# Optimization experiments

Measured on AMD Instinct MI355X. Metric: run time of the kernel, lower is better.

Reference implementation:

```python
import jax, jax.numpy as jnp
import numpy as np

NEG = -1e30  # safe -inf surrogate (keeps grads finite)
BLANK = 0
PRIOR_SCALE = 0.3


def prior_logsumexp(log_probs, input_lengths):
    # log_probs: [T, N, V]; logsumexp over all valid (t, n) frames -> [1, V]
    T = log_probs.shape[0]
    mask = jnp.arange(T)[:, None] < input_lengths[None, :]  # [T, N]
    masked = jnp.where(mask[:, :, None], log_probs, NEG)
    return jax.nn.logsumexp(masked, axis=(0, 1))[None, :]


def ctc_loss_mean(log_probs, targets, input_lengths, target_lengths):
    # Exact CTC forward (alpha) recursion, vectorized over batch, scanned over time.
    # log_probs: [T, N, V] (log scores), targets: [N, S] with values >= 1.
    T, N, V = log_probs.shape
    S = targets.shape[1]
    L = 2 * S + 1  # extended label sequence with interleaved blanks
    ext = jnp.full((N, L), BLANK, dtype=targets.dtype).at[:, 1::2].set(targets)
    # skip transition j-2 -> j allowed iff ext[j] != blank and ext[j] != ext[j-2]
    skip = jnp.zeros((N, L), bool).at[:, 2:].set(
        (ext[:, 2:] != BLANK) & (ext[:, 2:] != ext[:, :-2]))
    pad1 = jnp.full((N, 1), NEG, log_probs.dtype)
    pad2 = jnp.full((N, 2), NEG, log_probs.dtype)

    e0 = jnp.take_along_axis(log_probs[0], ext, axis=1)  # [N, L]
    alpha0 = (jnp.full((N, L), NEG, log_probs.dtype)
              .at[:, 0].set(e0[:, 0])
              .at[:, 1].set(e0[:, 1]))

    def step(alpha, xs):
        lp_t, t = xs
        emit = jnp.take_along_axis(lp_t, ext, axis=1)  # [N, L]
        s1 = jnp.concatenate([pad1, alpha[:, :-1]], axis=1)
        s2 = jnp.where(skip, jnp.concatenate([pad2, alpha[:, :-2]], axis=1), NEG)
        new = jax.nn.logsumexp(jnp.stack([alpha, s1, s2], 0), axis=0) + emit
        # freeze finished utterances (t >= input_length)
        alpha = jnp.where((t < input_lengths)[:, None], new, alpha)
        return alpha, None

    alpha, _ = jax.lax.scan(step, alpha0, (log_probs[1:], jnp.arange(1, T)))

    i1 = (2 * target_lengths)[:, None]
    a1 = jnp.take_along_axis(alpha, i1, axis=1)[:, 0]
    a2 = jnp.take_along_axis(alpha, i1 - 1, axis=1)[:, 0]
    ll = jnp.logaddexp(a1, a2)  # total log-likelihood per utterance
    # k2.ctc_loss(reduction='mean', target_lengths=...) == mean of (-ll / target_len)
    return jnp.mean(-ll / target_lengths.astype(log_probs.dtype))


def setup_inputs() -> dict:
    key = jax.random.key(0)
    k1, k2, k3, k4, k5 = jax.random.split(key, 5)
    T, N, V, S = 2000, 32, 256, 256
    log_probs = jax.nn.log_softmax(jax.random.normal(k1, (T, N, V), jnp.float32), axis=-1)
    log_priors = jax.nn.log_softmax(0.5 * jax.random.normal(k2, (1, V), jnp.float32), axis=-1)
    targets = jax.random.randint(k3, (N, S), 1, V)          # non-blank labels
    input_lengths = jax.random.randint(k4, (N,), T // 2, T + 1)
    target_lengths = jax.random.randint(k5, (N,), S // 2, S + 1)
    return {"log_probs": log_probs, "log_priors": log_priors, "targets": targets,
            "input_lengths": input_lengths, "target_lengths": target_lengths}


def reference(log_probs, log_priors, targets, input_lengths, target_lengths):
    # (1) detached label-prior accumulation pass (as in training step)
    log_batch_priors_sum = jax.lax.stop_gradient(prior_logsumexp(log_probs, input_lengths))
    # (2) prior-scaled log probs (log_priors broadcasts [1,V] -> [T,N,V])
    scaled = log_probs - PRIOR_SCALE * log_priors
    # (3) CTC forward-backward loss
    loss = ctc_loss_mean(scaled, targets, input_lengths, target_lengths)
    return loss, log_batch_priors_sum
```

## Files before the change

### kernel.cpp

```cpp
#include <hip/hip_runtime.h>

#define PRIOR_SCALE 0.3f
#define NEGF (-1e30f)
#define LOG2E_F 1.4426950408889634f
#define LN2_F 0.6931471805599453f
#define K_SS 8
#define MARG 24

#define PHASE_BARRIER() \
  asm volatile("s_waitcnt lgkmcnt(0)\n\ts_barrier" ::: "memory")

__device__ __forceinline__ float fexp2(float x) { return __builtin_amdgcn_exp2f(x); }
__device__ __forceinline__ float flog2(float x) { return __builtin_amdgcn_logf(x); }

__device__ __forceinline__ float lse2b(float a, float b) {
  float m = fmaxf(a, b);
  float d = fminf(a, b) - m;
  return m + flog2(1.0f + fexp2(d));
}

__device__ __forceinline__ float shr1_dpp(float x, float fill) {
  return __int_as_float(__builtin_amdgcn_update_dpp(
      __float_as_int(fill), __float_as_int(x), 0x138 , 0xF, 0xF, false));
}
__device__ __forceinline__ int shr1_dpp_i(int x, int fill) {
  return __builtin_amdgcn_update_dpp(fill, x, 0x138, 0xF, 0xF, false);
}
template <int CTRL, int RM>
__device__ __forceinline__ int dppi(int x) {
  return __builtin_amdgcn_update_dpp(x, x, CTRL, RM, 0xF, false);
}
__device__ __forceinline__ int imax2(int a, int b) { return a > b ? a : b; }

__device__ __forceinline__ void issue_pair(float& e, float& b, uint32_t offE,
                                           uint32_t offB, uint64_t base) {
  asm volatile("global_load_dword %0, %2, %4\n\t"
               "global_load_dword %1, %3, %4"
               : "=v"(e), "=v"(b)
               : "v"(offE), "v"(offB), "s"(base));
}
__device__ __forceinline__ void wait_pair(float& e, float& b) {
  asm volatile("s_waitcnt vmcnt(14)" : "+v"(e), "+v"(b));
}

extern "C" __global__ void __launch_bounds__(256, 1)
ctc_fused_kernel(const float* __restrict__ lp, const float* __restrict__ lpri,
                 const int* __restrict__ tgt, const int* __restrict__ ilen,
                 const int* __restrict__ tlen, float* __restrict__ nll,
                 float* __restrict__ partial, int pblocks,
                 int T, int N, int V, int S) {
  if ((int)blockIdx.x >= N) {
    const int pb = blockIdx.x - N;
    const int v = threadIdx.x;
    float s = 0.0f;
    for (int t = pb; t < T; t += pblocks) {
      const float* base = lp + (size_t)t * N * V + v;
      for (int nn = 0; nn < N; ++nn) {
        float x = base[(size_t)nn * V];
        s += (t < ilen[nn]) ? __expf(x) : 0.0f;
      }
    }
    partial[(size_t)pb * V + v] = s;
    return;
  }

  const int n = blockIdx.x;
  const int g = threadIdx.x;
  const int lane = g & 63;
  const int wid = __builtin_amdgcn_readfirstlane(threadIdx.x >> 6);
  __shared__ __align__(16) float mb[3][2048];
  __shared__ int mbe[3][256];
  __shared__ float afin[513];

  const int len = __builtin_amdgcn_readfirstlane(ilen[n]);
  const int tl = tlen[n];

  const int* trow = tgt + n * S;
  const int tv = trow[g];
  const int tvp = (g > 0) ? trow[g - 1] : -1;
  const float skf = (g > 0 && tv != tvp) ? 1.0f : 0.0f;
  const float ep1 = (-PRIOR_SCALE * lpri[tv]) * LOG2E_F;
  const float epb = (-PRIOR_SCALE * lpri[0]) * LOG2E_F;
  const int penB = MARG * ((lane & 15) + 1);
  const int penC = MARG * ((lane & 31) + 1);

  const float* rp = lp + (size_t)n * V;
  const uint32_t RBu = (uint32_t)(N * V * 4);
  const uint32_t tvb = (uint32_t)tv * 4u;
  const uint64_t gbase = (uint64_t)(uintptr_t)rp;

  float x0 = 0.0f, x1 = 0.0f, x2 = 0.0f;
  int e = 0;
  { float b0 = rp[0], e0 = rp[tv];
    if (g == 0) {
      x0 = fexp2(fmaf(b0, LOG2E_F, epb));
      x1 = fexp2(fmaf(e0, LOG2E_F, ep1));
    } }
  for (int idx = g; idx < 3 * 2048; idx += 256) ((float*)mb)[idx] = 0.0f;
  for (int idx = g; idx < 3 * 256; idx += 256) ((int*)mbe)[idx] = 0;

  float eR0, eR1, eR2, eR3, eR4, eR5, eR6, eR7;
  float bR0, bR1, bR2, bR3, bR4, bR5, bR6, bR7;
#define PRO(K) { uint32_t tt = (uint32_t)((1 + K < len) ? (1 + K) : (len - 1)); \
                 issue_pair(eR##K, bR##K, tt * RBu + tvb, tt * RBu, gbase); }
  PRO(0) PRO(1) PRO(2) PRO(3) PRO(4) PRO(5) PRO(6) PRO(7)
#undef PRO
  uint32_t ofB;
  { uint32_t tn = (uint32_t)((1 + K_SS < len) ? (1 + K_SS) : (len - 1));
    ofB = tn * RBu; }

  float mv0 = 0, mv1 = 0, mv2 = 0, mv3 = 0, mv4 = 0, mv5 = 0, mv6 = 0, mv7 = 0;

  PHASE_BARRIER();

  const int nss = (len - 1 + K_SS - 1) / K_SS;
  const int P = nss + 3;

#define STEP(KK, T_, DSC_) {                                                   \
    const int t = (T_);                                                        \
    if (t < len) {                                                             \
      wait_pair(eR##KK, bR##KK);                                               \
      float e1  = fexp2(fmaf(eR##KK, LOG2E_F, ep1));                           \
      float ebl = fexp2(fmaf(bR##KK, LOG2E_F, epb));                           \
      issue_pair(eR##KK, bR##KK, ofB + tvb, ofB, gbase);                       \
      ofB += ((t + 1 + K_SS) < len) ? RBu : 0u;                                \
      float am1 = ldexpf(shr1_dpp(x1, mv##KK), (DSC_));                        \
      am1 = fminf(am1, 1.0e33f);                         \
      float sel = (g == 255) ? x1 : 0.0f;                                      \
      float y0 = (x0 + am1) * ebl;                                             \
      float y1 = fmaf(skf, am1, x1 + x0) * e1;                                 \
      x2 = (x2 + sel) * ebl;                                                   \
      x0 = y0; x1 = y1;                                                        \
      if (lane == 63 && wid < 3) mb[wid][t] = y1;       \
    } }

  for (int p = 0; p < P; ++p) {
    const int i = p - wid;
    if (i >= 0 && i < nss) {
      const int t0 = 1 + i * K_SS;
      int eA = 0, eB = 0;
      if (wid > 0) {
        eB = mbe[wid - 1][i];
        eA = (i > 0) ? mbe[wid - 1][i - 1] : eB;
        const float4* mrow = (const float4*)&mb[wid - 1][t0 - 1];
        float4 q0 = mrow[0], q1 = mrow[1];
        mv0 = q0.x; mv1 = q0.y; mv2 = q0.z; mv3 = q0.w;
        mv4 = q1.x; mv5 = q1.y; mv6 = q1.z; mv7 = q1.w;
      }
      int dscL, dsc0;
      {
        float mxv = fmaxf(fmaxf(x0, x1), x2);
        int ex = (int)((__float_as_uint(mxv) >> 23) & 0xFFu) - 127;
        int ecand = (mxv > 0.0f) ? (e + ex - 40) : -2000000;
        if (wid > 0 && lane == 0) ecand = imax2(ecand, imax2(eA, eB) - MARG);
        int v = ecand;
        v = imax2(v, dppi<0x111, 0xF>(v) - MARG);
        v = imax2(v, dppi<0x112, 0xF>(v) - 2 * MARG);
        v = imax2(v, dppi<0x114, 0xF>(v) - 4 * MARG);
        v = imax2(v, dppi<0x118, 0xF>(v) - 8 * MARG);
        v = imax2(v, dppi<0x142, 0xA>(v) - penB);
        v = imax2(v, dppi<0x143, 0xC>(v) - penC);
        int dsc = e - v;
        x0 = ldexpf(x0, dsc);
        x1 = ldexpf(x1, dsc);
        x2 = ldexpf(x2, dsc);
        e = v;
        if (lane == 63 && wid < 3) mbe[wid][i] = e;
        int eprevL = shr1_dpp_i(e, eB);
        dscL = eprevL - e;
        dsc0 = (lane == 0) ? (eA - e) : dscL;
      }
      STEP(0, t0 + 0, dsc0)  STEP(1, t0 + 1, dscL)
      STEP(2, t0 + 2, dscL)  STEP(3, t0 + 3, dscL)
      STEP(4, t0 + 4, dscL)  STEP(5, t0 + 5, dscL)
      STEP(6, t0 + 6, dscL)  STEP(7, t0 + 7, dscL)
    }
    PHASE_BARRIER();
  }
#undef STEP

  asm volatile("s_waitcnt vmcnt(0)");
  asm volatile("" :: "v"(eR0), "v"(eR1), "v"(eR2), "v"(eR3),
                     "v"(eR4), "v"(eR5), "v"(eR6), "v"(eR7));
  asm volatile("" :: "v"(bR0), "v"(bR1), "v"(bR2), "v"(bR3),
                     "v"(bR4), "v"(bR5), "v"(bR6), "v"(bR7));

  const float ef = (float)e;
  afin[2 * g]     = fmaxf(flog2(x0) + ef, NEGF);
  afin[2 * g + 1] = fmaxf(flog2(x1) + ef, NEGF);
  if (g == 255) afin[512] = fmaxf(flog2(x2) + ef, NEGF);
  __syncthreads();
  if (g == 0) {
    const int i1 = 2 * tl;
    float ll = lse2b(afin[i1], afin[i1 - 1]) * LN2_F;
    nll[n] = -ll / (float)tl;
  }
}

extern "C" __global__ void finalize_kernel(const float* __restrict__ partial, int nstripes,
                                           const float* __restrict__ nll,
                                           float* __restrict__ out, int N, int V) {
  const int v = threadIdx.x;
  float s = 0.0f;
#pragma unroll 4
  for (int pb = 0; pb < nstripes; ++pb) s += partial[(size_t)pb * V + v];
  out[1 + v] = __logf(s);
  if (v == 0) {
    float acc = 0.0f;
#pragma unroll 8
    for (int i = 0; i < N; ++i) acc += nll[i];
    out[0] = acc / (float)N;
  }
}

extern "C" void kernel_launch(void* const* d_in, const int* in_sizes, int n_in,
                              void* d_out, int out_size, void* d_ws, size_t ws_size,
                              hipStream_t stream) {
  const float* lp   = (const float*)d_in[0];
  const float* lpri = (const float*)d_in[1];
  const int*   tgt  = (const int*)d_in[2];
  const int*   ilen = (const int*)d_in[3];
  const int*   tlen = (const int*)d_in[4];
  const int V = in_sizes[1];
  const int N = in_sizes[3];
  const int S = in_sizes[2] / N;
  const int T = in_sizes[0] / (N * V);

  int pblocks = 200;
  size_t need = ((size_t)pblocks * V + 64) * sizeof(float);
  if (ws_size < need) {
    long avail = (long)(ws_size / sizeof(float)) - 64;
    pblocks = (int)(avail / V);
    if (pblocks < 1) pblocks = 1;
  }

  float* out = (float*)d_out;
  float* partial = (float*)d_ws;
  float* nll = partial + (size_t)pblocks * V;

  ctc_fused_kernel<<<N + pblocks, 256, 0, stream>>>(lp, lpri, tgt, ilen, tlen,
                                                    nll, partial, pblocks, T, N, V, S);
  finalize_kernel<<<1, 256, 0, stream>>>(partial, pblocks, nll, out, N, V);
}
```

Measured before the change: 221.9 us.

## Precompute gathered emission exponentials in a parallel prep kernel before the serial scan

Adds a prep kernel that gathers the target-label and blank log-probs for every (n, t) and applies the prior scaling and exp2, storing them in a contiguous per-utterance workspace layout. The same kernel also does the prior logsumexp partial sums. The serial scan kernel then reads coalesced, precomputed emissions instead of doing strided gathers and exps on its critical path. The cost is an extra kernel launch and a large workspace write and read (N*T*256 floats), plus a two-stage finalize. The old fused kernel is kept as a fallback for when the workspace is too small.

```diff
diff --git a/kernel.cpp b/kernel.cpp
--- a/kernel.cpp
+++ b/kernel.cpp
@@ -6,6 +6,7 @@
 #define LN2_F 0.6931471805599453f
 #define K_SS 8
 #define MARG 24
+#define PB 512
 
 #define PHASE_BARRIER() \
   asm volatile("s_waitcnt lgkmcnt(0)\n\ts_barrier" ::: "memory")
@@ -43,27 +44,45 @@
   asm volatile("s_waitcnt vmcnt(14)" : "+v"(e), "+v"(b));
 }
 
+extern "C" __global__ void __launch_bounds__(256)
+prep_kernel(const float* __restrict__ lp, const float* __restrict__ lpri,
+            const int* __restrict__ tgt, const int* __restrict__ ilen,
+            float* __restrict__ Eodd, float* __restrict__ Ebl,
+            float* __restrict__ partial, int T, int N, int V, int S) {
+  const int tid = threadIdx.x;
+  const int b = blockIdx.x;
+  __shared__ int   stv[32 * 256];
+  __shared__ float spe[32 * 256];
+  __shared__ int   slen[32];
+  for (int idx = tid; idx < N * 256; idx += 256) {
+    int vv = tgt[idx];
+    stv[idx] = vv;
+    spe[idx] = (-PRIOR_SCALE * lpri[vv]) * LOG2E_F;
+  }
+  if (tid < N) slen[tid] = ilen[tid];
+  const float epb = (-PRIOR_SCALE * lpri[0]) * LOG2E_F;
+  __syncthreads();
+
+  float psum = 0.0f;
+  for (int t = b; t < T; t += PB) {
+#pragma unroll 2
+    for (int n = 0; n < 32; ++n) {
+      const float* row = lp + ((size_t)t * N + n) * V;
+      float val = row[tid];
+      if (t < slen[n]) psum += __expf(val);
+      float ev = row[stv[n * 256 + tid]];
+      Eodd[((size_t)n * T + t) * 256 + tid] =
+          fexp2(fmaf(ev, LOG2E_F, spe[n * 256 + tid]));
+      if (tid == 0) Ebl[(size_t)n * T + t] = fexp2(fmaf(row[0], LOG2E_F, epb));
+    }
+  }
+  partial[(size_t)b * 256 + tid] = psum;
+}
+
 extern "C" __global__ void __launch_bounds__(256, 1)
-ctc_fused_kernel(const float* __restrict__ lp, const float* __restrict__ lpri,
-                 const int* __restrict__ tgt, const int* __restrict__ ilen,
-                 const int* __restrict__ tlen, float* __restrict__ nll,
-                 float* __restrict__ partial, int pblocks,
-                 int T, int N, int V, int S) {
-  if ((int)blockIdx.x >= N) {
-    const int pb = blockIdx.x - N;
-    const int v = threadIdx.x;
-    float s = 0.0f;
-    for (int t = pb; t < T; t += pblocks) {
-      const float* base = lp + (size_t)t * N * V + v;
-      for (int nn = 0; nn < N; ++nn) {
-        float x = base[(size_t)nn * V];
-        s += (t < ilen[nn]) ? __expf(x) : 0.0f;
-      }
-    }
-    partial[(size_t)pb * V + v] = s;
-    return;
-  }
-
+ctc_scan_kernel(const float* __restrict__ ws_f, const int* __restrict__ tgt,
+                const int* __restrict__ ilen, const int* __restrict__ tlen,
+                float* __restrict__ nll, int T, int N, int S) {
   const int n = blockIdx.x;
   const int g = threadIdx.x;
   const int lane = g & 63;
@@ -79,35 +98,32 @@
   const int tv = trow[g];
   const int tvp = (g > 0) ? trow[g - 1] : -1;
   const float skf = (g > 0 && tv != tvp) ? 1.0f : 0.0f;
-  const float ep1 = (-PRIOR_SCALE * lpri[tv]) * LOG2E_F;
-  const float epb = (-PRIOR_SCALE * lpri[0]) * LOG2E_F;
   const int penB = MARG * ((lane & 15) + 1);
   const int penC = MARG * ((lane & 31) + 1);
 
-  const float* rp = lp + (size_t)n * V;
-  const uint32_t RBu = (uint32_t)(N * V * 4);
-  const uint32_t tvb = (uint32_t)tv * 4u;
-  const uint64_t gbase = (uint64_t)(uintptr_t)rp;
+  const float* eoddn = ws_f + (size_t)n * T * 256;
+  const uint64_t gbase = (uint64_t)(uintptr_t)eoddn;
+  const uint32_t eblOffB = (uint32_t)((((size_t)(N - n) * T) * 256 + (size_t)n * T) * 4);
+  const uint32_t gb4 = (uint32_t)g * 4u;
 
   float x0 = 0.0f, x1 = 0.0f, x2 = 0.0f;
   int e = 0;
-  { float b0 = rp[0], e0 = rp[tv];
-    if (g == 0) {
-      x0 = fexp2(fmaf(b0, LOG2E_F, epb));
-      x1 = fexp2(fmaf(e0, LOG2E_F, ep1));
-    } }
+  if (g == 0) {
+    x0 = ws_f[(size_t)N * T * 256 + (size_t)n * T];
+    x1 = eoddn[0];
+  }
   for (int idx = g; idx < 3 * 2048; idx += 256) ((float*)mb)[idx] = 0.0f;
   for (int idx = g; idx < 3 * 256; idx += 256) ((int*)mbe)[idx] = 0;
 
   float eR0, eR1, eR2, eR3, eR4, eR5, eR6, eR7;
   float bR0, bR1, bR2, bR3, bR4, bR5, bR6, bR7;
 #define PRO(K) { uint32_t tt = (uint32_t)((1 + K < len) ? (1 + K) : (len - 1)); \
-                 issue_pair(eR##K, bR##K, tt * RBu + tvb, tt * RBu, gbase); }
+                 issue_pair(eR##K, bR##K, tt * 1024u + gb4, eblOffB + tt * 4u, gbase); }
   PRO(0) PRO(1) PRO(2) PRO(3) PRO(4) PRO(5) PRO(6) PRO(7)
 #undef PRO
-  uint32_t ofB;
+  uint32_t ofE, ofBl;
   { uint32_t tn = (uint32_t)((1 + K_SS < len) ? (1 + K_SS) : (len - 1));
-    ofB = tn * RBu; }
+    ofE = tn * 1024u; ofBl = eblOffB + tn * 4u; }
 
   float mv0 = 0, mv1 = 0, mv2 = 0, mv3 = 0, mv4 = 0, mv5 = 0, mv6 = 0, mv7 = 0;
 
@@ -120,10 +136,12 @@
     const int t = (T_);                                                        \
     if (t < len) {                                                             \
       wait_pair(eR##KK, bR##KK);                                               \
-      float e1  = fexp2(fmaf(eR##KK, LOG2E_F, ep1));                           \
-      float ebl = fexp2(fmaf(bR##KK, LOG2E_F, epb));                           \
-      issue_pair(eR##KK, bR##KK, ofB + tvb, ofB, gbase);                       \
-      ofB += ((t + 1 + K_SS) < len) ? RBu : 0u;                                \
+      float e1  = eR##KK;                                                      \
+      float ebl = bR##KK;                                                      \
+      issue_pair(eR##KK, bR##KK, ofE + gb4, ofBl, gbase);                      \
+      bool adv = ((t + 1 + K_SS) < len);                                       \
+      ofE  += adv ? 1024u : 0u;                                                \
+      ofBl += adv ? 4u : 0u;                                                   \
       float am1 = ldexpf(shr1_dpp(x1, mv##KK), (DSC_));                        \
       am1 = fminf(am1, 1.0e33f);                         \
       float sel = (g == 255) ? x1 : 0.0f;                                      \
@@ -197,6 +215,171 @@
   }
 }
 
+extern "C" __global__ void __launch_bounds__(256)
+finalize1_kernel(const float* __restrict__ partial, float* __restrict__ partial2) {
+  const int v = threadIdx.x;
+  const int b = blockIdx.x;
+  float s = 0.0f;
+#pragma unroll 4
+  for (int pb = b; pb < PB; pb += 32) s += partial[(size_t)pb * 256 + v];
+  partial2[(size_t)b * 256 + v] = s;
+}
+extern "C" __global__ void __launch_bounds__(256)
+finalize2_kernel(const float* __restrict__ partial2, const float* __restrict__ nll,
+                 float* __restrict__ out, int N) {
+  const int v = threadIdx.x;
+  float s = 0.0f;
+#pragma unroll
+  for (int b = 0; b < 32; ++b) s += partial2[(size_t)b * 256 + v];
+  out[1 + v] = __logf(s);
+  if (v == 0) {
+    float acc = 0.0f;
+#pragma unroll 8
+    for (int i = 0; i < N; ++i) acc += nll[i];
+    out[0] = acc / (float)N;
+  }
+}
+
+extern "C" __global__ void __launch_bounds__(256, 1)
+ctc_fused_r12(const float* __restrict__ lp, const float* __restrict__ lpri,
+              const int* __restrict__ tgt, const int* __restrict__ ilen,
+              const int* __restrict__ tlen, float* __restrict__ nll,
+              float* __restrict__ partial, int pblocks,
+              int T, int N, int V, int S) {
+  if ((int)blockIdx.x >= N) {
+    const int pb = blockIdx.x - N;
+    const int v = threadIdx.x;
+    float s = 0.0f;
+    for (int t = pb; t < T; t += pblocks) {
+      const float* base = lp + (size_t)t * N * V + v;
+      for (int nn = 0; nn < N; ++nn) {
+        float x = base[(size_t)nn * V];
+        s += (t < ilen[nn]) ? __expf(x) : 0.0f;
+      }
+    }
+    partial[(size_t)pb * V + v] = s;
+    return;
+  }
+  const int n = blockIdx.x;
+  const int g = threadIdx.x;
+  const int lane = g & 63;
+  const int wid = __builtin_amdgcn_readfirstlane(threadIdx.x >> 6);
+  __shared__ __align__(16) float mb[3][2048];
+  __shared__ int mbe[3][256];
+  __shared__ float afin[513];
+  const int len = __builtin_amdgcn_readfirstlane(ilen[n]);
+  const int tl = tlen[n];
+  const int* trow = tgt + n * S;
+  const int tv = trow[g];
+  const int tvp = (g > 0) ? trow[g - 1] : -1;
+  const float skf = (g > 0 && tv != tvp) ? 1.0f : 0.0f;
+  const float ep1 = (-PRIOR_SCALE * lpri[tv]) * LOG2E_F;
+  const float epb = (-PRIOR_SCALE * lpri[0]) * LOG2E_F;
+  const int penB = MARG * ((lane & 15) + 1);
+  const int penC = MARG * ((lane & 31) + 1);
+  const float* rp = lp + (size_t)n * V;
+  const uint32_t RBu = (uint32_t)(N * V * 4);
+  const uint32_t tvb = (uint32_t)tv * 4u;
+  const uint64_t gbase = (uint64_t)(uintptr_t)rp;
+  float x0 = 0.0f, x1 = 0.0f, x2 = 0.0f;
+  int e = 0;
+  { float b0 = rp[0], e0 = rp[tv];
+    if (g == 0) {
+      x0 = fexp2(fmaf(b0, LOG2E_F, epb));
+      x1 = fexp2(fmaf(e0, LOG2E_F, ep1));
+    } }
+  for (int idx = g; idx < 3 * 2048; idx += 256) ((float*)mb)[idx] = 0.0f;
+  for (int idx = g; idx < 3 * 256; idx += 256) ((int*)mbe)[idx] = 0;
+  float eR0, eR1, eR2, eR3, eR4, eR5, eR6, eR7;
+  float bR0, bR1, bR2, bR3, bR4, bR5, bR6, bR7;
+#define PRO(K) { uint32_t tt = (uint32_t)((1 + K < len) ? (1 + K) : (len - 1)); \
+                 issue_pair(eR##K, bR##K, tt * RBu + tvb, tt * RBu, gbase); }
+  PRO(0) PRO(1) PRO(2) PRO(3) PRO(4) PRO(5) PRO(6) PRO(7)
+#undef PRO
+  uint32_t ofB;
+  { uint32_t tn = (uint32_t)((1 + K_SS < len) ? (1 + K_SS) : (len - 1));
+    ofB = tn * RBu; }
+  float mv0 = 0, mv1 = 0, mv2 = 0, mv3 = 0, mv4 = 0, mv5 = 0, mv6 = 0, mv7 = 0;
+  PHASE_BARRIER();
+  const int nss = (len - 1 + K_SS - 1) / K_SS;
+  const int P = nss + 3;
+#define STEP(KK, T_, DSC_) {                                                   \
+    const int t = (T_);                                                        \
+    if (t < len) {                                                             \
+      wait_pair(eR##KK, bR##KK);                                               \
+      float e1  = fexp2(fmaf(eR##KK, LOG2E_F, ep1));                           \
+      float ebl = fexp2(fmaf(bR##KK, LOG2E_F, epb));                           \
+      issue_pair(eR##KK, bR##KK, ofB + tvb, ofB, gbase);                       \
+      ofB += ((t + 1 + K_SS) < len) ? RBu : 0u;                                \
+      float am1 = ldexpf(shr1_dpp(x1, mv##KK), (DSC_));                        \
+      am1 = fminf(am1, 1.0e33f);                                               \
+      float sel = (g == 255) ? x1 : 0.0f;                                      \
+      float y0 = (x0 + am1) * ebl;                                             \
+      float y1 = fmaf(skf, am1, x1 + x0) * e1;                                 \
+      x2 = (x2 + sel) * ebl;                                                   \
+      x0 = y0; x1 = y1;                                                        \
+      if (lane == 63 && wid < 3) mb[wid][t] = y1;                              \
+    } }
+  for (int p = 0; p < P; ++p) {
+    const int i = p - wid;
+    if (i >= 0 && i < nss) {
+      const int t0 = 1 + i * K_SS;
+      int eA = 0, eB = 0;
+      if (wid > 0) {
+        eB = mbe[wid - 1][i];
+        eA = (i > 0) ? mbe[wid - 1][i - 1] : eB;
+        const float4* mrow = (const float4*)&mb[wid - 1][t0 - 1];
+        float4 q0 = mrow[0], q1 = mrow[1];
+        mv0 = q0.x; mv1 = q0.y; mv2 = q0.z; mv3 = q0.w;
+        mv4 = q1.x; mv5 = q1.y; mv6 = q1.z; mv7 = q1.w;
+      }
+      int dscL, dsc0;
+      {
+        float mxv = fmaxf(fmaxf(x0, x1), x2);
+        int ex = (int)((__float_as_uint(mxv) >> 23) & 0xFFu) - 127;
+        int ecand = (mxv > 0.0f) ? (e + ex - 40) : -2000000;
+        if (wid > 0 && lane == 0) ecand = imax2(ecand, imax2(eA, eB) - MARG);
+        int v = ecand;
+        v = imax2(v, dppi<0x111, 0xF>(v) - MARG);
+        v = imax2(v, dppi<0x112, 0xF>(v) - 2 * MARG);
+        v = imax2(v, dppi<0x114, 0xF>(v) - 4 * MARG);
+        v = imax2(v, dppi<0x118, 0xF>(v) - 8 * MARG);
+        v = imax2(v, dppi<0x142, 0xA>(v) - penB);
+        v = imax2(v, dppi<0x143, 0xC>(v) - penC);
+        int dsc = e - v;
+        x0 = ldexpf(x0, dsc);
+        x1 = ldexpf(x1, dsc);
+        x2 = ldexpf(x2, dsc);
+        e = v;
+        if (lane == 63 && wid < 3) mbe[wid][i] = e;
+        int eprevL = shr1_dpp_i(e, eB);
+        dscL = eprevL - e;
+        dsc0 = (lane == 0) ? (eA - e) : dscL;
+      }
+      STEP(0, t0 + 0, dsc0)  STEP(1, t0 + 1, dscL)
+      STEP(2, t0 + 2, dscL)  STEP(3, t0 + 3, dscL)
+      STEP(4, t0 + 4, dscL)  STEP(5, t0 + 5, dscL)
+      STEP(6, t0 + 6, dscL)  STEP(7, t0 + 7, dscL)
+    }
+    PHASE_BARRIER();
+  }
+#undef STEP
+  asm volatile("s_waitcnt vmcnt(0)");
+  asm volatile("" :: "v"(eR0), "v"(eR1), "v"(eR2), "v"(eR3),
+                     "v"(eR4), "v"(eR5), "v"(eR6), "v"(eR7));
+  asm volatile("" :: "v"(bR0), "v"(bR1), "v"(bR2), "v"(bR3),
+                     "v"(bR4), "v"(bR5), "v"(bR6), "v"(bR7));
+  const float ef = (float)e;
+  afin[2 * g]     = fmaxf(flog2(x0) + ef, NEGF);
+  afin[2 * g + 1] = fmaxf(flog2(x1) + ef, NEGF);
+  if (g == 255) afin[512] = fmaxf(flog2(x2) + ef, NEGF);
+  __syncthreads();
+  if (g == 0) {
+    const int i1 = 2 * tl;
+    float ll = lse2b(afin[i1], afin[i1 - 1]) * LN2_F;
+    nll[n] = -ll / (float)tl;
+  }
+}
 extern "C" __global__ void finalize_kernel(const float* __restrict__ partial, int nstripes,
                                            const float* __restrict__ nll,
                                            float* __restrict__ out, int N, int V) {
@@ -226,19 +409,37 @@
   const int S = in_sizes[2] / N;
   const int T = in_sizes[0] / (N * V);
 
-  int pblocks = 200;
-  size_t need = ((size_t)pblocks * V + 64) * sizeof(float);
-  if (ws_size < need) {
-    long avail = (long)(ws_size / sizeof(float)) - 64;
-    pblocks = (int)(avail / V);
-    if (pblocks < 1) pblocks = 1;
-  }
-
   float* out = (float*)d_out;
-  float* partial = (float*)d_ws;
-  float* nll = partial + (size_t)pblocks * V;
-
-  ctc_fused_kernel<<<N + pblocks, 256, 0, stream>>>(lp, lpri, tgt, ilen, tlen,
-                                                    nll, partial, pblocks, T, N, V, S);
-  finalize_kernel<<<1, 256, 0, stream>>>(partial, pblocks, nll, out, N, V);
-}
+
+  const size_t eodd_f = (size_t)N * T * 256;
+  const size_t ebl_f  = (size_t)N * T;
+  const size_t need = (eodd_f + ebl_f + (size_t)PB * 256 + 32 * 256 + N) * sizeof(float);
+
+  if (ws_size >= need) {
+    float* ws_f     = (float*)d_ws;
+    float* Eodd     = ws_f;
+    float* Ebl      = ws_f + eodd_f;
+    float* partial  = Ebl + ebl_f;
+    float* partial2 = partial + (size_t)PB * 256;
+    float* nll      = partial2 + 32 * 256;
+
+    prep_kernel<<<PB, 256, 0, stream>>>(lp, lpri, tgt, ilen, Eodd, Ebl,
+                                        partial, T, N, V, S);
+    ctc_scan_kernel<<<N, 256, 0, stream>>>(ws_f, tgt, ilen, tlen, nll, T, N, S);
+    finalize1_kernel<<<32, 256, 0, stream>>>(partial, partial2);
+    finalize2_kernel<<<1, 256, 0, stream>>>(partial2, nll, out, N);
+  } else {
+    int pblocks = 200;
+    size_t need2 = ((size_t)pblocks * V + 64) * sizeof(float);
+    if (ws_size < need2) {
+      long avail = (long)(ws_size / sizeof(float)) - 64;
+      pblocks = (int)(avail / V);
+      if (pblocks < 1) pblocks = 1;
+    }
+    float* partial = (float*)d_ws;
+    float* nll = partial + (size_t)pblocks * V;
+    ctc_fused_r12<<<N + pblocks, 256, 0, stream>>>(lp, lpri, tgt, ilen, tlen,
+                                                   nll, partial, pblocks, T, N, V, S);
+    finalize_kernel<<<1, 256, 0, stream>>>(partial, pblocks, nll, out, N, V);
+  }
+}
```

Measured after the change: 282.3 us. +27.2%, slower.
